# Optimization experiments

Measured on AMD Instinct MI355X. Metric: run time of the kernel, lower is better.

The kernel has to match this reference:

```python
import jax, jax.numpy as jnp
import numpy as np

N_HEADS = 32
N_KV = 8
HEAD_DIM = 128
BLOCK_SIZE = 16
MAX_SEQ = 2048
ROPE_BASE = 10000.0
SCALE = HEAD_DIM ** -0.5


def _rope(x, pos):
    # x: [B, H, head_dim], pos: [B] int32 -> half-split (non-traditional) RoPE
    half = HEAD_DIM // 2
    inv_freq = 1.0 / (ROPE_BASE ** (jnp.arange(half, dtype=jnp.float32) / half))
    ang = pos.astype(jnp.float32)[:, None] * inv_freq[None, :]      # [B, half]
    c = jnp.cos(ang)[:, None, :]
    s = jnp.sin(ang)[:, None, :]
    x1, x2 = x[..., :half], x[..., half:]
    return jnp.concatenate([x1 * c - x2 * s, x1 * s + x2 * c], axis=-1)


def setup_inputs() -> dict:
    key = jax.random.key(0)
    ks = jax.random.split(key, 9)
    B, D = 32, 4096
    max_blocks = MAX_SEQ // BLOCK_SIZE  # 128
    num_blocks = B * max_blocks         # 4096 -> 65536 slots
    sc = 1.0 / np.sqrt(D)
    inp = {
        "x": jax.random.normal(ks[0], (B, 1, D), jnp.float32),
        "Wq": jax.random.normal(ks[1], (D, N_HEADS * HEAD_DIM), jnp.float32) * sc,
        "Wk": jax.random.normal(ks[2], (D, N_KV * HEAD_DIM), jnp.float32) * sc,
        "Wv": jax.random.normal(ks[3], (D, N_KV * HEAD_DIM), jnp.float32) * sc,
        "Wo": jax.random.normal(ks[4], (N_HEADS * HEAD_DIM, D), jnp.float32) * sc,
        "key_cache": jax.random.normal(ks[5], (num_blocks * BLOCK_SIZE, N_KV, HEAD_DIM), jnp.float32),
        "value_cache": jax.random.normal(ks[6], (num_blocks * BLOCK_SIZE, N_KV, HEAD_DIM), jnp.float32),
        # disjoint valid block tables per request
        "block_tables": jnp.arange(num_blocks, dtype=jnp.int32).reshape(B, max_blocks),
        "context_lens": jax.random.randint(ks[7], (B,), 1, MAX_SEQ + 1, jnp.int32),
    }
    return inp


def reference(x, Wq, Wk, Wv, Wo, key_cache, value_cache, block_tables, context_lens):
    B = x.shape[0]
    G = N_HEADS // N_KV  # GQA group size
    xb = x[:, 0, :]  # [B, D] (L=1 decode)

    q = (xb @ Wq).reshape(B, N_HEADS, HEAD_DIM)
    k = (xb @ Wk).reshape(B, N_KV, HEAD_DIM)
    v = (xb @ Wv).reshape(B, N_KV, HEAD_DIM)

    # per-request RoPE at offset = position of the new token
    pos = context_lens - 1  # [B]
    q = _rope(q, pos)
    k = _rope(k, pos)

    # reshape_and_cache: scatter new K/V into paged caches via slot mapping
    new_slot = block_tables[jnp.arange(B), pos // BLOCK_SIZE] * BLOCK_SIZE + pos % BLOCK_SIZE  # [B]
    key_cache = key_cache.at[new_slot].set(k)
    value_cache = value_cache.at[new_slot].set(v)

    # paged_attention_v1: gather K/V through block tables, masked softmax attention
    t = jnp.arange(MAX_SEQ, dtype=jnp.int32)                        # [S]
    slots = block_tables[:, t // BLOCK_SIZE] * BLOCK_SIZE + t % BLOCK_SIZE  # [B, S]
    K = key_cache[slots]    # [B, S, N_KV, HEAD_DIM]
    V = value_cache[slots]  # [B, S, N_KV, HEAD_DIM]

    qg = q.reshape(B, N_KV, G, HEAD_DIM)
    scores = jnp.einsum("bkgd,bskd->bkgs", qg, K) * SCALE           # [B, N_KV, G, S]
    valid = t[None, :] < context_lens[:, None]                      # [B, S]
    scores = jnp.where(valid[:, None, None, :], scores, jnp.float32(-1e30))
    p = jax.nn.softmax(scores, axis=-1)
    out = jnp.einsum("bkgs,bskd->bkgd", p, V).reshape(B, N_HEADS * HEAD_DIM)

    return (out @ Wo).reshape(B, 1, -1)
```

## Files before the change

kernel.cpp:

```cpp
#include <hip/hip_runtime.h>
#include <hip/hip_bf16.h>
#include <math.h>

#define BATCH   32
#define DIM     4096
#define NH      32
#define NKV     8
#define GQ      4
#define HD      128
#define BS      16
#define MAXSEQ  2048
#define NBLK_TBL 128
#define SCALE_F 0.08838834764831845f

#define CHUNK_D   128
#define NCHUNK_D  32
#define ATT_CHUNK 256
#define ATT_NCHUNK 8
#define ATT_TILE  32
#define QKV_COLS  6144

__global__ __launch_bounds__(256) void gemm_split(
    const float* __restrict__ X,
    const float* __restrict__ W0, int ld0, int n0,
    const float* __restrict__ W1, int ld1, int n1,
    const float* __restrict__ W2, int ld2, int n2,
    int OT, float* __restrict__ partial)
{
    __shared__ float xs[BATCH][CHUNK_D];
    const int tid = threadIdx.x;
    const int colbase = blockIdx.x * 128;
    const int d0 = blockIdx.y * CHUNK_D;

    #pragma unroll
    for (int rep = 0; rep < 4; ++rep) {
        int f4 = rep * 256 + tid;
        int b  = f4 >> 5;
        int j  = (f4 & 31) << 2;
        *(float4*)&xs[b][j] = *(const float4*)(X + b * DIM + d0 + j);
    }
    __syncthreads();

    const float* W; int ld, off;
    if (colbase < n0)           { W = W0; ld = ld0; off = colbase; }
    else if (colbase < n0 + n1) { W = W1; ld = ld1; off = colbase - n0; }
    else                        { W = W2; ld = ld2; off = colbase - n0 - n1; }

    const int colgrp = tid & 31;
    const int bgrp   = tid >> 5;
    const float* Wp = W + off + colgrp * 4;

    float acc[4][4];
    #pragma unroll
    for (int i = 0; i < 4; ++i)
        #pragma unroll
        for (int j = 0; j < 4; ++j) acc[i][j] = 0.f;

    for (int j4 = 0; j4 < CHUNK_D / 4; ++j4) {
        const int d = d0 + j4 * 4;
        float4 w0 = *(const float4*)(Wp + (size_t)(d + 0) * ld);
        float4 w1 = *(const float4*)(Wp + (size_t)(d + 1) * ld);
        float4 w2 = *(const float4*)(Wp + (size_t)(d + 2) * ld);
        float4 w3 = *(const float4*)(Wp + (size_t)(d + 3) * ld);
        #pragma unroll
        for (int bb = 0; bb < 4; ++bb) {
            float4 xv = *(const float4*)&xs[bgrp * 4 + bb][j4 * 4];
            acc[bb][0] += xv.x * w0.x + xv.y * w1.x + xv.z * w2.x + xv.w * w3.x;
            acc[bb][1] += xv.x * w0.y + xv.y * w1.y + xv.z * w2.y + xv.w * w3.y;
            acc[bb][2] += xv.x * w0.z + xv.y * w1.z + xv.z * w2.z + xv.w * w3.z;
            acc[bb][3] += xv.x * w0.w + xv.y * w1.w + xv.z * w2.w + xv.w * w3.w;
        }
    }

    const int chunk = blockIdx.y;
    #pragma unroll
    for (int bb = 0; bb < 4; ++bb) {
        int b = bgrp * 4 + bb;
        float4 o = make_float4(acc[bb][0], acc[bb][1], acc[bb][2], acc[bb][3]);
        *(float4*)(partial + ((size_t)chunk * BATCH + b) * OT + colbase + colgrp * 4) = o;
    }
}

__global__ __launch_bounds__(256) void rope_cache_update(
    const float* __restrict__ qkvp,
    const int* __restrict__ ctxlen, const int* __restrict__ btab,
    float* __restrict__ q_out,
    float* __restrict__ kcache, float* __restrict__ vcache)
{
    __shared__ float buf[1024];
    const int b = blockIdx.x, seg = blockIdx.y, tid = threadIdx.x;
    const int cbase = seg * 1024;
    for (int c = tid; c < 1024; c += 256) {
        float s = 0.f;
        #pragma unroll
        for (int ch = 0; ch < NCHUNK_D; ++ch)
            s += qkvp[((size_t)ch * BATCH + b) * QKV_COLS + cbase + c];
        buf[c] = s;
    }
    __syncthreads();
    const int pos  = ctxlen[b] - 1;
    const int slot = btab[b * NBLK_TBL + (pos >> 4)] * BS + (pos & 15);
    const float fpos = (float)pos;
    const float NEG_LN_BASE_OVER_HALF = -0.14391156831212787f;

    if (seg < 4) {
        for (int p = tid; p < 8 * 64; p += 256) {
            int h = p >> 6, i = p & 63;
            float x1 = buf[h * HD + i];
            float x2 = buf[h * HD + i + 64];
            float ang = fpos * __expf(NEG_LN_BASE_OVER_HALF * (float)i);
            float sn, cs;
            __sincosf(ang, &sn, &cs);
            q_out[b * 4096 + cbase + h * HD + i]      = x1 * cs - x2 * sn;
            q_out[b * 4096 + cbase + h * HD + i + 64] = x1 * sn + x2 * cs;
        }
    } else if (seg == 4) {
        for (int p = tid; p < NKV * 64; p += 256) {
            int kv = p >> 6, i = p & 63;
            float x1 = buf[kv * HD + i];
            float x2 = buf[kv * HD + i + 64];
            float ang = fpos * __expf(NEG_LN_BASE_OVER_HALF * (float)i);
            float sn, cs;
            __sincosf(ang, &sn, &cs);
            kcache[((size_t)slot * NKV + kv) * HD + i]      = x1 * cs - x2 * sn;
            kcache[((size_t)slot * NKV + kv) * HD + i + 64] = x1 * sn + x2 * cs;
        }
    } else {
        for (int p = tid; p < NKV * HD; p += 256) {
            int kv = p >> 7, i = p & 127;
            vcache[((size_t)slot * NKV + kv) * HD + i] = buf[p];
        }
    }
}

__global__ __launch_bounds__(256) void attn_partial(
    const float* __restrict__ q,
    const float* __restrict__ kcache, const float* __restrict__ vcache,
    const int* __restrict__ btab, const int* __restrict__ ctxlen,
    float* __restrict__ part)
{
    const int b = blockIdx.x, kv = blockIdx.y, c = blockIdx.z;
    const int tid = threadIdx.x;
    const int ctx = ctxlen[b];
    const int start = c * ATT_CHUNK;
    const int end = min(ctx, start + ATT_CHUNK);
    float* pp = part + ((size_t)(b * NKV + kv) * ATT_NCHUNK + c) * (4 * 132);
    if (start >= end) {
        for (int i = tid; i < 4 * 132; i += 256) {
            int r = i - (i / 132) * 132;
            pp[i] = (r == 128) ? -1e30f : 0.f;
        }
        return;
    }
    __shared__ float Ks[ATT_TILE][132];
    __shared__ float Vs[ATT_TILE][128];
    __shared__ float qs[4][HD];
    __shared__ float p_lds[4][ATT_TILE];

    for (int i = tid; i < 4 * HD; i += 256)
        qs[i >> 7][i & 127] = q[b * 4096 + kv * GQ * HD + i];

    const int h    = tid >> 6;
    const int lane = tid & 63;

    float m_run = -1e30f, l_run = 0.f;
    float2 oacc = make_float2(0.f, 0.f);

    for (int t0 = start; t0 < end; t0 += ATT_TILE) {
        const int nt = min(ATT_TILE, end - t0);
        for (int idx = tid; idx < nt * 32; idx += 256) {
            int tt = idx >> 5, f4 = idx & 31;
            int tok = t0 + tt;
            int slot = btab[b * NBLK_TBL + (tok >> 4)] * BS + (tok & 15);
            size_t base = ((size_t)slot * NKV + kv) * HD + f4 * 4;
            *(float4*)&Ks[tt][f4 * 4] = *(const float4*)(kcache + base);
            *(float4*)&Vs[tt][f4 * 4] = *(const float4*)(vcache + base);
        }
        __syncthreads();

        float s = -1e30f;
        if (lane < nt) {
            float sum = 0.f;
            #pragma unroll
            for (int d4 = 0; d4 < 32; ++d4) {
                float4 kk = *(const float4*)&Ks[lane][d4 * 4];
                float4 qq = *(const float4*)&qs[h][d4 * 4];
                sum += kk.x * qq.x + kk.y * qq.y + kk.z * qq.z + kk.w * qq.w;
            }
            s = sum * SCALE_F;
        }
        float mt = s;
        #pragma unroll
        for (int off = 1; off < 64; off <<= 1)
            mt = fmaxf(mt, __shfl_xor(mt, off));
        float mn = fmaxf(m_run, mt);
        float al = __expf(m_run - mn);
        float p  = (lane < nt) ? __expf(s - mn) : 0.f;
        float ps = p;
        #pragma unroll
        for (int off = 1; off < 64; off <<= 1)
            ps += __shfl_xor(ps, off);
        l_run = l_run * al + ps;
        m_run = mn;
        p_lds[h][lane & (ATT_TILE - 1)] = p;
        if (lane < ATT_TILE) p_lds[h][lane] = p;

        oacc.x *= al; oacc.y *= al;
        for (int t = 0; t < nt; ++t) {
            float pv = p_lds[h][t];
            float2 vv = *(const float2*)&Vs[t][lane * 2];
            oacc.x += pv * vv.x; oacc.y += pv * vv.y;
        }
        __syncthreads();
    }
    *(float2*)(pp + h * 132 + lane * 2) = oacc;
    if (lane == 0) {
        pp[h * 132 + 128] = m_run;
        pp[h * 132 + 129] = l_run;
    }
}

__global__ __launch_bounds__(128) void attn_reduce(
    const float* __restrict__ part, float* __restrict__ attn_out)
{
    const int b = blockIdx.x, kv = blockIdx.y;
    const int d = threadIdx.x;
    const float* base = part + (size_t)(b * NKV + kv) * ATT_NCHUNK * (4 * 132);
    #pragma unroll
    for (int h = 0; h < 4; ++h) {
        float M = -1e30f;
        #pragma unroll
        for (int c2 = 0; c2 < ATT_NCHUNK; ++c2)
            M = fmaxf(M, base[c2 * (4 * 132) + h * 132 + 128]);
        float L = 0.f, o = 0.f;
        #pragma unroll
        for (int c2 = 0; c2 < ATT_NCHUNK; ++c2) {
            float m = base[c2 * (4 * 132) + h * 132 + 128];
            float l = base[c2 * (4 * 132) + h * 132 + 129];
            float w = __expf(m - M);
            L += l * w;
            o += base[c2 * (4 * 132) + h * 132 + d] * w;
        }
        attn_out[b * 4096 + (kv * GQ + h) * HD + d] = o / L;
    }
}

__global__ __launch_bounds__(256) void final_reduce(
    const float* __restrict__ part, float* __restrict__ out)
{
    const int b = blockIdx.x;
    const int cb = blockIdx.y * 1024;
    for (int c = threadIdx.x; c < 1024; c += 256) {
        float s = 0.f;
        #pragma unroll
        for (int ch = 0; ch < NCHUNK_D; ++ch)
            s += part[((size_t)ch * BATCH + b) * DIM + cb + c];
        out[b * DIM + cb + c] = s;
    }
}

extern "C" void kernel_launch(void* const* d_in, const int* in_sizes, int n_in,
                              void* d_out, int out_size, void* d_ws, size_t ws_size,
                              hipStream_t stream)
{
    const float* x  = (const float*)d_in[0];
    const float* Wq = (const float*)d_in[1];
    const float* Wk = (const float*)d_in[2];
    const float* Wv = (const float*)d_in[3];
    const float* Wo = (const float*)d_in[4];
    float* kc = (float*)d_in[5];
    float* vc = (float*)d_in[6];
    const int* bt  = (const int*)d_in[7];
    const int* ctx = (const int*)d_in[8];
    float* out = (float*)d_out;

    float* ws = (float*)d_ws;
    float* qkvp      = ws;
    float* q_ws      = qkvp + (size_t)NCHUNK_D * BATCH * QKV_COLS;
    float* attn_part = q_ws + (size_t)BATCH * 4096;
    float* attn_o    = attn_part + (size_t)BATCH * NKV * ATT_NCHUNK * 4 * 132;
    float* oprojp    = attn_o + (size_t)BATCH * 4096;

    gemm_split<<<dim3(48, NCHUNK_D), 256, 0, stream>>>(
        x, Wq, 4096, 4096, Wk, 1024, 1024, Wv, 1024, 1024, QKV_COLS, qkvp);
    rope_cache_update<<<dim3(32, 6), 256, 0, stream>>>(qkvp, ctx, bt, q_ws, kc, vc);
    attn_partial<<<dim3(BATCH, NKV, ATT_NCHUNK), 256, 0, stream>>>(
        q_ws, kc, vc, bt, ctx, attn_part);
    attn_reduce<<<dim3(BATCH, NKV), 128, 0, stream>>>(attn_part, attn_o);
    gemm_split<<<dim3(32, NCHUNK_D), 256, 0, stream>>>(
        attn_o, Wo, 4096, 4096, nullptr, 0, 0, nullptr, 0, 0, DIM, oprojp);
    final_reduce<<<dim3(32, 4), 256, 0, stream>>>(oprojp, out);
}
```

Before: 669.1 us.

## Prefetch GEMM weights, bypass paged cache write, split QK dot across half-waves

Adds register double-buffering of weight rows in the split-K GEMM so the next rows load while the current ones are consumed. The new K/V token is written to a small workspace instead of the paged cache, and attention reads it from there when it reaches the current position. The QK dot product is split across two half-waves so all lanes are busy, and the PV loop is unrolled with two accumulators. Empty attention chunks no longer write partials, and the reduce loops only over valid chunks. The in-place cache update is no longer performed, which changes side effects on the input caches.

```diff
diff --git a/kernel.cpp b/kernel.cpp
--- a/kernel.cpp
+++ b/kernel.cpp
@@ -56,12 +56,20 @@
         #pragma unroll
         for (int j = 0; j < 4; ++j) acc[i][j] = 0.f;
 
+    float4 w0 = *(const float4*)(Wp + (size_t)(d0 + 0) * ld);
+    float4 w1 = *(const float4*)(Wp + (size_t)(d0 + 1) * ld);
+    float4 w2 = *(const float4*)(Wp + (size_t)(d0 + 2) * ld);
+    float4 w3 = *(const float4*)(Wp + (size_t)(d0 + 3) * ld);
+
     for (int j4 = 0; j4 < CHUNK_D / 4; ++j4) {
-        const int d = d0 + j4 * 4;
-        float4 w0 = *(const float4*)(Wp + (size_t)(d + 0) * ld);
-        float4 w1 = *(const float4*)(Wp + (size_t)(d + 1) * ld);
-        float4 w2 = *(const float4*)(Wp + (size_t)(d + 2) * ld);
-        float4 w3 = *(const float4*)(Wp + (size_t)(d + 3) * ld);
+        float4 n0, n1, n2, n3;
+        if (j4 + 1 < CHUNK_D / 4) {
+            const int dn = d0 + (j4 + 1) * 4;
+            n0 = *(const float4*)(Wp + (size_t)(dn + 0) * ld);
+            n1 = *(const float4*)(Wp + (size_t)(dn + 1) * ld);
+            n2 = *(const float4*)(Wp + (size_t)(dn + 2) * ld);
+            n3 = *(const float4*)(Wp + (size_t)(dn + 3) * ld);
+        } else { n0 = w0; n1 = w1; n2 = w2; n3 = w3; }
         #pragma unroll
         for (int bb = 0; bb < 4; ++bb) {
             float4 xv = *(const float4*)&xs[bgrp * 4 + bb][j4 * 4];
@@ -70,6 +78,7 @@
             acc[bb][2] += xv.x * w0.z + xv.y * w1.z + xv.z * w2.z + xv.w * w3.z;
             acc[bb][3] += xv.x * w0.w + xv.y * w1.w + xv.z * w2.w + xv.w * w3.w;
         }
+        w0 = n0; w1 = n1; w2 = n2; w3 = n3;
     }
 
     const int chunk = blockIdx.y;
@@ -81,11 +90,12 @@
     }
 }
 
-__global__ __launch_bounds__(256) void rope_cache_update(
+__global__ __launch_bounds__(256) void rope_qkv(
     const float* __restrict__ qkvp,
-    const int* __restrict__ ctxlen, const int* __restrict__ btab,
+    const int* __restrict__ ctxlen,
     float* __restrict__ q_out,
-    float* __restrict__ kcache, float* __restrict__ vcache)
+    float* __restrict__ knew,
+    float* __restrict__ vnew)
 {
     __shared__ float buf[1024];
     const int b = blockIdx.x, seg = blockIdx.y, tid = threadIdx.x;
@@ -99,7 +109,6 @@
     }
     __syncthreads();
     const int pos  = ctxlen[b] - 1;
-    const int slot = btab[b * NBLK_TBL + (pos >> 4)] * BS + (pos & 15);
     const float fpos = (float)pos;
     const float NEG_LN_BASE_OVER_HALF = -0.14391156831212787f;
 
@@ -122,36 +131,30 @@
             float ang = fpos * __expf(NEG_LN_BASE_OVER_HALF * (float)i);
             float sn, cs;
             __sincosf(ang, &sn, &cs);
-            kcache[((size_t)slot * NKV + kv) * HD + i]      = x1 * cs - x2 * sn;
-            kcache[((size_t)slot * NKV + kv) * HD + i + 64] = x1 * sn + x2 * cs;
+            knew[((size_t)b * NKV + kv) * HD + i]      = x1 * cs - x2 * sn;
+            knew[((size_t)b * NKV + kv) * HD + i + 64] = x1 * sn + x2 * cs;
         }
     } else {
-        for (int p = tid; p < NKV * HD; p += 256) {
-            int kv = p >> 7, i = p & 127;
-            vcache[((size_t)slot * NKV + kv) * HD + i] = buf[p];
-        }
+        for (int p = tid; p < NKV * HD; p += 256)
+            vnew[(size_t)b * NKV * HD + p] = buf[p];
     }
 }
 
 __global__ __launch_bounds__(256) void attn_partial(
     const float* __restrict__ q,
+    const float* __restrict__ knew, const float* __restrict__ vnew,
     const float* __restrict__ kcache, const float* __restrict__ vcache,
     const int* __restrict__ btab, const int* __restrict__ ctxlen,
     float* __restrict__ part)
 {
     const int b = blockIdx.x, kv = blockIdx.y, c = blockIdx.z;
-    const int tid = threadIdx.x;
     const int ctx = ctxlen[b];
     const int start = c * ATT_CHUNK;
+    if (start >= ctx) return;
     const int end = min(ctx, start + ATT_CHUNK);
-    float* pp = part + ((size_t)(b * NKV + kv) * ATT_NCHUNK + c) * (4 * 132);
-    if (start >= end) {
-        for (int i = tid; i < 4 * 132; i += 256) {
-            int r = i - (i / 132) * 132;
-            pp[i] = (r == 128) ? -1e30f : 0.f;
-        }
-        return;
-    }
+    const int pos = ctx - 1;
+    const int tid = threadIdx.x;
+
     __shared__ float Ks[ATT_TILE][132];
     __shared__ float Vs[ATT_TILE][128];
     __shared__ float qs[4][HD];
@@ -162,58 +165,82 @@
 
     const int h    = tid >> 6;
     const int lane = tid & 63;
+    const int t_l  = lane & 31;
+    const int half = lane >> 5;
 
     float m_run = -1e30f, l_run = 0.f;
-    float2 oacc = make_float2(0.f, 0.f);
+    float2 oa = make_float2(0.f, 0.f);
+    float2 ob = make_float2(0.f, 0.f);
 
     for (int t0 = start; t0 < end; t0 += ATT_TILE) {
         const int nt = min(ATT_TILE, end - t0);
         for (int idx = tid; idx < nt * 32; idx += 256) {
             int tt = idx >> 5, f4 = idx & 31;
             int tok = t0 + tt;
-            int slot = btab[b * NBLK_TBL + (tok >> 4)] * BS + (tok & 15);
-            size_t base = ((size_t)slot * NKV + kv) * HD + f4 * 4;
-            *(float4*)&Ks[tt][f4 * 4] = *(const float4*)(kcache + base);
-            *(float4*)&Vs[tt][f4 * 4] = *(const float4*)(vcache + base);
+            const float* ksrc; const float* vsrc;
+            if (tok == pos) {
+                size_t nb = ((size_t)b * NKV + kv) * HD;
+                ksrc = knew + nb; vsrc = vnew + nb;
+            } else {
+                int slot = btab[b * NBLK_TBL + (tok >> 4)] * BS + (tok & 15);
+                size_t base = ((size_t)slot * NKV + kv) * HD;
+                ksrc = kcache + base; vsrc = vcache + base;
+            }
+            *(float4*)&Ks[tt][f4 * 4] = *(const float4*)(ksrc + f4 * 4);
+            *(float4*)&Vs[tt][f4 * 4] = *(const float4*)(vsrc + f4 * 4);
         }
         __syncthreads();
 
-        float s = -1e30f;
-        if (lane < nt) {
-            float sum = 0.f;
+        float sum = 0.f;
+        {
+            const float* kr = &Ks[t_l][half * 64];
+            const float* qr = &qs[h][half * 64];
             #pragma unroll
-            for (int d4 = 0; d4 < 32; ++d4) {
-                float4 kk = *(const float4*)&Ks[lane][d4 * 4];
-                float4 qq = *(const float4*)&qs[h][d4 * 4];
+            for (int d4 = 0; d4 < 16; ++d4) {
+                float4 kk = *(const float4*)(kr + d4 * 4);
+                float4 qq = *(const float4*)(qr + d4 * 4);
                 sum += kk.x * qq.x + kk.y * qq.y + kk.z * qq.z + kk.w * qq.w;
             }
-            s = sum * SCALE_F;
-        }
+        }
+        sum += __shfl_xor(sum, 32);
+        float s = (t_l < nt) ? sum * SCALE_F : -1e30f;
+
         float mt = s;
         #pragma unroll
-        for (int off = 1; off < 64; off <<= 1)
+        for (int off = 1; off < 32; off <<= 1)
             mt = fmaxf(mt, __shfl_xor(mt, off));
         float mn = fmaxf(m_run, mt);
         float al = __expf(m_run - mn);
-        float p  = (lane < nt) ? __expf(s - mn) : 0.f;
+        float p  = (t_l < nt) ? __expf(s - mn) : 0.f;
         float ps = p;
         #pragma unroll
-        for (int off = 1; off < 64; off <<= 1)
+        for (int off = 1; off < 32; off <<= 1)
             ps += __shfl_xor(ps, off);
         l_run = l_run * al + ps;
         m_run = mn;
-        p_lds[h][lane & (ATT_TILE - 1)] = p;
         if (lane < ATT_TILE) p_lds[h][lane] = p;
 
-        oacc.x *= al; oacc.y *= al;
-        for (int t = 0; t < nt; ++t) {
-            float pv = p_lds[h][t];
-            float2 vv = *(const float2*)&Vs[t][lane * 2];
-            oacc.x += pv * vv.x; oacc.y += pv * vv.y;
+        oa.x *= al; oa.y *= al; ob.x *= al; ob.y *= al;
+        if (nt == ATT_TILE) {
+            #pragma unroll
+            for (int t = 0; t < ATT_TILE; t += 2) {
+                float p0 = p_lds[h][t], p1 = p_lds[h][t + 1];
+                float2 v0 = *(const float2*)&Vs[t][lane * 2];
+                float2 v1 = *(const float2*)&Vs[t + 1][lane * 2];
+                oa.x += p0 * v0.x; oa.y += p0 * v0.y;
+                ob.x += p1 * v1.x; ob.y += p1 * v1.y;
+            }
+        } else {
+            for (int t = 0; t < nt; ++t) {
+                float pv = p_lds[h][t];
+                float2 vv = *(const float2*)&Vs[t][lane * 2];
+                oa.x += pv * vv.x; oa.y += pv * vv.y;
+            }
         }
         __syncthreads();
     }
-    *(float2*)(pp + h * 132 + lane * 2) = oacc;
+    float* pp = part + ((size_t)(b * NKV + kv) * ATT_NCHUNK + c) * (4 * 132);
+    *(float2*)(pp + h * 132 + lane * 2) = make_float2(oa.x + ob.x, oa.y + ob.y);
     if (lane == 0) {
         pp[h * 132 + 128] = m_run;
         pp[h * 132 + 129] = l_run;
@@ -221,20 +248,20 @@
 }
 
 __global__ __launch_bounds__(128) void attn_reduce(
-    const float* __restrict__ part, float* __restrict__ attn_out)
+    const float* __restrict__ part, const int* __restrict__ ctxlen,
+    float* __restrict__ attn_out)
 {
     const int b = blockIdx.x, kv = blockIdx.y;
     const int d = threadIdx.x;
+    const int nc = (ctxlen[b] + ATT_CHUNK - 1) / ATT_CHUNK;
     const float* base = part + (size_t)(b * NKV + kv) * ATT_NCHUNK * (4 * 132);
     #pragma unroll
     for (int h = 0; h < 4; ++h) {
         float M = -1e30f;
-        #pragma unroll
-        for (int c2 = 0; c2 < ATT_NCHUNK; ++c2)
+        for (int c2 = 0; c2 < nc; ++c2)
             M = fmaxf(M, base[c2 * (4 * 132) + h * 132 + 128]);
         float L = 0.f, o = 0.f;
-        #pragma unroll
-        for (int c2 = 0; c2 < ATT_NCHUNK; ++c2) {
+        for (int c2 = 0; c2 < nc; ++c2) {
             float m = base[c2 * (4 * 132) + h * 132 + 128];
             float l = base[c2 * (4 * 132) + h * 132 + 129];
             float w = __expf(m - M);
@@ -268,8 +295,8 @@
     const float* Wk = (const float*)d_in[2];
     const float* Wv = (const float*)d_in[3];
     const float* Wo = (const float*)d_in[4];
-    float* kc = (float*)d_in[5];
-    float* vc = (float*)d_in[6];
+    const float* kc = (const float*)d_in[5];
+    const float* vc = (const float*)d_in[6];
     const int* bt  = (const int*)d_in[7];
     const int* ctx = (const int*)d_in[8];
     float* out = (float*)d_out;
@@ -277,16 +304,18 @@
     float* ws = (float*)d_ws;
     float* qkvp      = ws;
     float* q_ws      = qkvp + (size_t)NCHUNK_D * BATCH * QKV_COLS;
-    float* attn_part = q_ws + (size_t)BATCH * 4096;
+    float* knew      = q_ws + (size_t)BATCH * 4096;
+    float* vnew      = knew + (size_t)BATCH * NKV * HD;
+    float* attn_part = vnew + (size_t)BATCH * NKV * HD;
     float* attn_o    = attn_part + (size_t)BATCH * NKV * ATT_NCHUNK * 4 * 132;
     float* oprojp    = attn_o + (size_t)BATCH * 4096;
 
     gemm_split<<<dim3(48, NCHUNK_D), 256, 0, stream>>>(
         x, Wq, 4096, 4096, Wk, 1024, 1024, Wv, 1024, 1024, QKV_COLS, qkvp);
-    rope_cache_update<<<dim3(32, 6), 256, 0, stream>>>(qkvp, ctx, bt, q_ws, kc, vc);
+    rope_qkv<<<dim3(32, 6), 256, 0, stream>>>(qkvp, ctx, q_ws, knew, vnew);
     attn_partial<<<dim3(BATCH, NKV, ATT_NCHUNK), 256, 0, stream>>>(
-        q_ws, kc, vc, bt, ctx, attn_part);
-    attn_reduce<<<dim3(BATCH, NKV), 128, 0, stream>>>(attn_part, attn_o);
+        q_ws, knew, vnew, kc, vc, bt, ctx, attn_part);
+    attn_reduce<<<dim3(BATCH, NKV), 128, 0, stream>>>(attn_part, ctx, attn_o);
     gemm_split<<<dim3(32, NCHUNK_D), 256, 0, stream>>>(
         attn_o, Wo, 4096, 4096, nullptr, 0, 0, nullptr, 0, 0, DIM, oprojp);
     final_reduce<<<dim3(32, 4), 256, 0, stream>>>(oprojp, out);
```

After: 673.7 us. Within noise of the previous version (+0.7%).
